# Kernel optimization log

Hardware: AMD Instinct MI355X
Metric: run time of the kernel (lower is better)

## Reference

```python
import jax, jax.numpy as jnp
import numpy as np

B, K, T, D, NH, HD, DFF, L = 2, 512, 2048, 1024, 16, 64, 4096, 2
EPS = 1e-5


def rotate_half(x):
    x1, x2 = jnp.split(x, 2, axis=-1)
    return jnp.concatenate([-x2, x1], axis=-1)


def rmsnorm(x, w):
    return x * jax.lax.rsqrt(jnp.mean(x * x, axis=-1, keepdims=True) + EPS) * w


def setup_inputs():
    key = jax.random.key(0)
    ks = jax.random.split(key, 16)
    x_processed = jax.random.normal(ks[0], (B, K, D), jnp.float32)
    # counts[b] = number of chunks n; boundaries[b, :n-1] = ascending chunk ends in (0, T),
    # positions >= n-1 padded with T (sentinel, never used by the original loop).
    counts = jax.random.randint(ks[1], (B,), K // 2, K + 1)
    raw = jnp.sort(jax.random.randint(ks[2], (B, K), 1, T), axis=1)
    j = jnp.arange(K)[None, :]
    boundaries = jnp.where(j < counts[:, None] - 1, raw, T)
    x_residual = jax.random.normal(ks[3], (B, T, D), jnp.float32)
    inv_freq = 1.0 / (10000.0 ** (jnp.arange(0, HD, 2, dtype=jnp.float32) / HD))
    freqs = jnp.arange(T, dtype=jnp.float32)[:, None] * inv_freq[None, :]  # [T, HD//2]
    emb = jnp.concatenate([freqs, freqs], axis=-1)                          # [T, HD]
    cos, sin = jnp.cos(emb), jnp.sin(emb)
    s = 0.02
    wq = jax.random.normal(ks[4], (L, D, D), jnp.float32) * s
    wk = jax.random.normal(ks[5], (L, D, D), jnp.float32) * s
    wv = jax.random.normal(ks[6], (L, D, D), jnp.float32) * s
    wo = jax.random.normal(ks[7], (L, D, D), jnp.float32) * s
    w1 = jax.random.normal(ks[8], (L, D, DFF), jnp.float32) * s
    w3 = jax.random.normal(ks[9], (L, D, DFF), jnp.float32) * s
    w2 = jax.random.normal(ks[10], (L, DFF, D), jnp.float32) * s
    attn_norm_w = jnp.ones((L, D), jnp.float32)
    mlp_norm_w = jnp.ones((L, D), jnp.float32)
    final_norm_w = jnp.ones((D,), jnp.float32)
    return {"x_processed": x_processed, "boundaries": boundaries, "counts": counts,
            "x_residual": x_residual, "cos": cos, "sin": sin, "seq_len": T,
            "wq": wq, "wk": wk, "wv": wv, "wo": wo,
            "attn_norm_w": attn_norm_w, "mlp_norm_w": mlp_norm_w,
            "w1": w1, "w3": w3, "w2": w2, "final_norm_w": final_norm_w}


def reference(x_processed, boundaries, counts, x_residual, cos, sin, seq_len,
              wq, wk, wv, wo, attn_norm_w, mlp_norm_w, w1, w3, w2, final_norm_w):
    Bn, Kn, Dn = x_processed.shape
    Tn = x_residual.shape[1]
    # Vectorized chunk expansion: token t belongs to chunk i = #{boundaries <= t}
    # (boundaries ascending; entries beyond n-1 are padded with seq_len so they never count).
    t = jnp.arange(Tn)
    idx = jax.vmap(lambda row: jnp.searchsorted(row, t, side='right'))(boundaries)  # [B, T]
    x = jnp.take_along_axis(x_processed, idx[:, :, None], axis=1) + x_residual     # [B, T, D]

    mask = jnp.tril(jnp.ones((Tn, Tn), dtype=bool))
    scale = 1.0 / jnp.sqrt(jnp.float32(HD))
    c = cos[None, :, None, :]
    s = sin[None, :, None, :]
    for l in range(L):
        h = rmsnorm(x, attn_norm_w[l])
        q = (h @ wq[l]).reshape(Bn, Tn, NH, HD)
        k = (h @ wk[l]).reshape(Bn, Tn, NH, HD)
        v = (h @ wv[l]).reshape(Bn, Tn, NH, HD)
        q = q * c + rotate_half(q) * s
        k = k * c + rotate_half(k) * s
        scores = jnp.einsum('bthd,bshd->bhts', q, k) * scale
        scores = jnp.where(mask[None, None], scores, -jnp.inf)
        probs = jax.nn.softmax(scores, axis=-1)
        o = jnp.einsum('bhts,bshd->bthd', probs, v).reshape(Bn, Tn, Dn)
        x = x + o @ wo[l]
        h = rmsnorm(x, mlp_norm_w[l])
        x = x + (jax.nn.silu(h @ w1[l]) * (h @ w3[l])) @ w2[l]
    return rmsnorm(x, final_norm_w)
```

## Files before the change

### kernel.cpp

```cpp
#include <hip/hip_runtime.h>
#include <stdint.h>

typedef __attribute__((ext_vector_type(8))) short s16x8;
typedef __attribute__((ext_vector_type(4))) float f32x4;

#define CB 2
#define CT 2048
#define CD 1024
#define CNH 16
#define CHD 64
#define CDFF 4096
#define CKB 512

__device__ __forceinline__ short f2bf(float f){
  union { float f; uint32_t u; } v; v.f = f;
  uint32_t r = v.u + 0x7FFFu + ((v.u >> 16) & 1u);
  return (short)(r >> 16);
}
__device__ __forceinline__ float bf2f(short h){
  union { uint32_t u; float f; } v; v.u = ((uint32_t)(uint16_t)h) << 16;
  return v.f;
}
__device__ __forceinline__ uint32_t cvtpk_bf16(float lo, float hi){
  uint32_t r;
  asm("v_cvt_pk_bf16_f32 %0, %1, %2" : "=v"(r) : "v"(lo), "v"(hi));
  return r;
}

#define GLOAD16(g, l) __builtin_amdgcn_global_load_lds( \
    (const __attribute__((address_space(1))) void*)(g), \
    (__attribute__((address_space(3))) void*)(l), 16, 0, 0)

__global__ void gather_kernel(const float* __restrict__ xp, const int* __restrict__ bnd,
                              const float* __restrict__ xr, float* __restrict__ x){
  int t = blockIdx.x, b = blockIdx.y, tid = threadIdx.x;
  int lo = 0, hi = CKB;
  while (lo < hi){ int mid = (lo + hi) >> 1; if (bnd[b*CKB + mid] <= t) lo = mid + 1; else hi = mid; }
  const float4* s  = (const float4*)(xp + ((size_t)b*CKB + lo)*CD);
  const float4* rr = (const float4*)(xr + ((size_t)b*CT + t)*CD);
  float4* dst      = (float4*)(x  + ((size_t)b*CT + t)*CD);
  float4 a = s[tid], c = rr[tid];
  float4 o; o.x = a.x + c.x; o.y = a.y + c.y; o.z = a.z + c.z; o.w = a.w + c.w;
  dst[tid] = o;
}

__global__ void wtrans_kernel(const float* __restrict__ W, short* __restrict__ dst,
                              int Kd, int Nd){
  __shared__ __align__(16) float tile[64*65];
  int n0 = blockIdx.x*64, k0 = blockIdx.y*64;
  #pragma unroll
  for (int i = 0; i < 16; ++i){
    int e = threadIdx.x + 256*i; int kl = e >> 6, nl = e & 63;
    tile[kl*65 + nl] = W[(size_t)(k0 + kl)*Nd + n0 + nl];
  }
  __syncthreads();
  #pragma unroll
  for (int i = 0; i < 16; ++i){
    int e = threadIdx.x + 256*i; int nl = e >> 6, kl = e & 63;
    dst[(size_t)(n0 + nl)*Kd + k0 + kl] = f2bf(tile[kl*65 + nl]);
  }
}

__global__ void wtrans_inter_kernel(const float* __restrict__ W, short* __restrict__ dst,
                                    int Kd, int Nd, int off16){
  __shared__ __align__(16) float tile[64*65];
  int n0 = blockIdx.x*64, k0 = blockIdx.y*64;
  #pragma unroll
  for (int i = 0; i < 16; ++i){
    int e = threadIdx.x + 256*i; int kl = e >> 6, nl = e & 63;
    tile[kl*65 + nl] = W[(size_t)(k0 + kl)*Nd + n0 + nl];
  }
  __syncthreads();
  #pragma unroll
  for (int i = 0; i < 16; ++i){
    int e = threadIdx.x + 256*i; int nl = e >> 6, kl = e & 63;
    int c = n0 + nl;
    int frow = ((c >> 4) << 5) + off16 + (c & 15);
    dst[(size_t)frow*Kd + k0 + kl] = f2bf(tile[kl*65 + nl]);
  }
}

template<int OUT_BF16>
__global__ void rmsnorm_kernel(const float* __restrict__ x, const float* __restrict__ w,
                               void* __restrict__ outv){
  int row = blockIdx.x, tid = threadIdx.x;
  const float4 xv = ((const float4*)(x + (size_t)row*CD))[tid];
  float ss = xv.x*xv.x + xv.y*xv.y + xv.z*xv.z + xv.w*xv.w;
  #pragma unroll
  for (int m = 1; m < 64; m <<= 1) ss += __shfl_xor(ss, m);
  __shared__ float red[4];
  if ((tid & 63) == 0) red[tid >> 6] = ss;
  __syncthreads();
  float tot = red[0] + red[1] + red[2] + red[3];
  float scale = rsqrtf(tot * (1.0f/1024.0f) + 1e-5f);
  const float4 wv = ((const float4*)w)[tid];
  if (OUT_BF16){
    short4 o;
    o.x = f2bf(xv.x*scale*wv.x); o.y = f2bf(xv.y*scale*wv.y);
    o.z = f2bf(xv.z*scale*wv.z); o.w = f2bf(xv.w*scale*wv.w);
    ((short4*)outv)[(size_t)row*256 + tid] = o;
  } else {
    float4 o;
    o.x = xv.x*scale*wv.x; o.y = xv.y*scale*wv.y;
    o.z = xv.z*scale*wv.z; o.w = xv.w*scale*wv.w;
    ((float4*)outv)[(size_t)row*256 + tid] = o;
  }
}

__device__ __forceinline__ void swz_block_id(int id, int NX, int NY, int& bm, int& bn){
  const int nwg = NX*NY;
  const int qq = nwg >> 3, rr8 = nwg & 7;
  const int xcd = id & 7, loc = id >> 3;
  const int wgid = (xcd < rr8 ? xcd*(qq+1) : rr8*(qq+1) + (xcd-rr8)*qq) + loc;
  const int GM = 8;
  const int gsz = GM * NX;
  const int gidg = wgid / gsz;
  const int remg = wgid - gidg*gsz;
  bm = gidg*GM + (remg % GM);
  bn = remg / GM;
}

template<int EPI>
__global__ __launch_bounds__(256) void gemm_bt(const short* __restrict__ A,
                                               const short* __restrict__ Bt,
                                               void* __restrict__ Cv,
                                               int M, int N, int K,
                                               int NX, int NY){
  __shared__ __align__(16) short sA[2][128*32];
  __shared__ __align__(16) short sB[2][128*32];
  const int tid = threadIdx.x;
  const int lane = tid & 63, wid = tid >> 6;
  const int wm = wid >> 1, wn = wid & 1;
  const int lr = lane & 15, lg = lane >> 4;
  int bm, bn; swz_block_id(blockIdx.x, NX, NY, bm, bn);
  const int bm0 = bm * 128, bn0 = bn * 128;

  f32x4 acc[4][4];
  #pragma unroll
  for (int i = 0; i < 4; ++i)
    #pragma unroll
    for (int j = 0; j < 4; ++j) acc[i][j] = (f32x4){0.f,0.f,0.f,0.f};

  const short* gA = A  + (size_t)(bm0 + wid*32 + (lane >> 2))*K + (lane & 3)*8;
  const short* gB = Bt + (size_t)(bn0 + wid*32 + (lane >> 2))*K + (lane & 3)*8;

  #pragma unroll
  for (int iss = 0; iss < 2; ++iss){
    GLOAD16(gA + (size_t)iss*16*K, &sA[0][wid*1024 + iss*16*32]);
    GLOAD16(gB + (size_t)iss*16*K, &sB[0][wid*1024 + iss*16*32]);
  }
  __syncthreads();

  int cur = 0;
  for (int k0 = 0; k0 < K; k0 += 32){
    if (k0 + 32 < K){
      #pragma unroll
      for (int iss = 0; iss < 2; ++iss){
        GLOAD16(gA + (size_t)iss*16*K + k0 + 32, &sA[cur^1][wid*1024 + iss*16*32]);
        GLOAD16(gB + (size_t)iss*16*K + k0 + 32, &sB[cur^1][wid*1024 + iss*16*32]);
      }
    }
    s16x8 af[4], bq[4];
    #pragma unroll
    for (int i = 0; i < 4; ++i) af[i] = *(const s16x8*)&sA[cur][(wm*64 + i*16 + lr)*32 + lg*8];
    #pragma unroll
    for (int j = 0; j < 4; ++j) bq[j] = *(const s16x8*)&sB[cur][(wn*64 + j*16 + lr)*32 + lg*8];
    #pragma unroll
    for (int i = 0; i < 4; ++i)
      #pragma unroll
      for (int j = 0; j < 4; ++j)
        acc[i][j] = __builtin_amdgcn_mfma_f32_16x16x32_bf16(af[i], bq[j], acc[i][j], 0, 0, 0);
    __syncthreads();
    cur ^= 1;
  }

  if (EPI == 0){
    short* C = (short*)Cv;
    #pragma unroll
    for (int i = 0; i < 4; ++i){
      int row0 = bm0 + wm*64 + i*16 + lg*4;
      #pragma unroll
      for (int j = 0; j < 4; ++j){
        int col = bn0 + wn*64 + j*16 + lr;
        #pragma unroll
        for (int r = 0; r < 4; ++r) C[(size_t)(row0 + r)*N + col] = f2bf(acc[i][j][r]);
      }
    }
  } else {
    float* C = (float*)Cv;
    #pragma unroll
    for (int i = 0; i < 4; ++i){
      int row0 = bm0 + wm*64 + i*16 + lg*4;
      #pragma unroll
      for (int j = 0; j < 4; ++j){
        int col = bn0 + wn*64 + j*16 + lr;
        #pragma unroll
        for (int r = 0; r < 4; ++r) C[(size_t)(row0 + r)*N + col] += acc[i][j][r];
      }
    }
  }
}

__global__ __launch_bounds__(256) void gemm_splitk(const short* __restrict__ A,
                                                   const short* __restrict__ Bt,
                                                   float* __restrict__ Cp,
                                                   int M, int N, int Ktot, int Kchunk,
                                                   int NX, int NY){
  __shared__ __align__(16) short sA[2][128*32];
  __shared__ __align__(16) short sB[2][128*32];
  const int tid = threadIdx.x;
  const int lane = tid & 63, wid = tid >> 6;
  const int wm = wid >> 1, wn = wid & 1;
  const int lr = lane & 15, lg = lane >> 4;
  const int nin = NX*NY;
  const int split = blockIdx.x / nin;
  const int inner = blockIdx.x - split*nin;
  int bm, bn; swz_block_id(inner, NX, NY, bm, bn);
  const int bm0 = bm * 128, bn0 = bn * 128;
  const int koff = split * Kchunk;

  f32x4 acc[4][4];
  #pragma unroll
  for (int i = 0; i < 4; ++i)
    #pragma unroll
    for (int j = 0; j < 4; ++j) acc[i][j] = (f32x4){0.f,0.f,0.f,0.f};

  const short* gA = A  + (size_t)(bm0 + wid*32 + (lane >> 2))*Ktot + koff + (lane & 3)*8;
  const short* gB = Bt + (size_t)(bn0 + wid*32 + (lane >> 2))*Ktot + koff + (lane & 3)*8;

  #pragma unroll
  for (int iss = 0; iss < 2; ++iss){
    GLOAD16(gA + (size_t)iss*16*Ktot, &sA[0][wid*1024 + iss*16*32]);
    GLOAD16(gB + (size_t)iss*16*Ktot, &sB[0][wid*1024 + iss*16*32]);
  }
  __syncthreads();

  int cur = 0;
  for (int k0 = 0; k0 < Kchunk; k0 += 32){
    if (k0 + 32 < Kchunk){
      #pragma unroll
      for (int iss = 0; iss < 2; ++iss){
        GLOAD16(gA + (size_t)iss*16*Ktot + k0 + 32, &sA[cur^1][wid*1024 + iss*16*32]);
        GLOAD16(gB + (size_t)iss*16*Ktot + k0 + 32, &sB[cur^1][wid*1024 + iss*16*32]);
      }
    }
    s16x8 af[4], bq[4];
    #pragma unroll
    for (int i = 0; i < 4; ++i) af[i] = *(const s16x8*)&sA[cur][(wm*64 + i*16 + lr)*32 + lg*8];
    #pragma unroll
    for (int j = 0; j < 4; ++j) bq[j] = *(const s16x8*)&sB[cur][(wn*64 + j*16 + lr)*32 + lg*8];
    #pragma unroll
    for (int i = 0; i < 4; ++i)
      #pragma unroll
      for (int j = 0; j < 4; ++j)
        acc[i][j] = __builtin_amdgcn_mfma_f32_16x16x32_bf16(af[i], bq[j], acc[i][j], 0, 0, 0);
    __syncthreads();
    cur ^= 1;
  }

  float* C = Cp + (size_t)split*M*N;
  #pragma unroll
  for (int i = 0; i < 4; ++i){
    int row0 = bm0 + wm*64 + i*16 + lg*4;
    #pragma unroll
    for (int j = 0; j < 4; ++j){
      int col = bn0 + wn*64 + j*16 + lr;
      #pragma unroll
      for (int r = 0; r < 4; ++r) C[(size_t)(row0 + r)*N + col] = acc[i][j][r];
    }
  }
}

__global__ void redadd_kernel(float* __restrict__ x, const float* __restrict__ Cp){
  size_t i = (size_t)blockIdx.x*256 + threadIdx.x;
  const float4* p0 = (const float4*)Cp;
  const float4* p1 = p0 + (size_t)1048576;
  const float4* p2 = p1 + (size_t)1048576;
  const float4* p3 = p2 + (size_t)1048576;
  float4 a = ((float4*)x)[i];
  float4 q0 = p0[i], q1 = p1[i], q2 = p2[i], q3 = p3[i];
  a.x += (q0.x + q1.x) + (q2.x + q3.x);
  a.y += (q0.y + q1.y) + (q2.y + q3.y);
  a.z += (q0.z + q1.z) + (q2.z + q3.z);
  a.w += (q0.w + q1.w) + (q2.w + q3.w);
  ((float4*)x)[i] = a;
}

#define STAGE8(u, kt, bufx) do { \
  const short* Gp_ = ((u)&1) ? Bt : A; \
  const int rb_ = ((u)&1) ? bn0 : bm0; \
  const int kh_ = (u)>>1; \
  _Pragma("unroll") \
  for (int L_ = 0; L_ < 2; ++L_){ \
    int rowS_ = L_*128 + wid*16 + (lane>>2); \
    int sp_ = (lane&3) ^ ((rowS_>>1)&3); \
    GLOAD16(Gp_ + (size_t)(rb_ + rowS_)*K + (size_t)(kt)*64 + kh_*32 + sp_*8, \
            &sAB[bufx][u][(L_*512 + wid*64)*8]); \
  } \
} while(0)

#define PHASE8(p, ch, kk) do { \
  if (pf) STAGE8(p, kt+1, nbuf); \
  s16x8 af_[4], bq_[4]; \
  _Pragma("unroll") \
  for (int ii_ = 0; ii_ < 4; ++ii_){ \
    int rowA_ = wm*128 + ((ch)*4 + ii_)*16 + lr; \
    af_[ii_] = *(const s16x8*)&sAB[buf][(kk)*2][rowA_*32 + ((lg ^ ((rowA_>>1)&3))<<3)]; \
  } \
  _Pragma("unroll") \
  for (int j_ = 0; j_ < 4; ++j_){ \
    int rowB_ = wn*64 + j_*16 + lr; \
    bq_[j_] = *(const s16x8*)&sAB[buf][(kk)*2+1][rowB_*32 + ((lg ^ ((rowB_>>1)&3))<<3)]; \
  } \
  __builtin_amdgcn_s_barrier(); \
  asm volatile("s_waitcnt lgkmcnt(0)" ::: "memory"); \
  __builtin_amdgcn_s_setprio(1); \
  _Pragma("unroll") \
  for (int ii_ = 0; ii_ < 4; ++ii_) \
    _Pragma("unroll") \
    for (int j_ = 0; j_ < 4; ++j_) \
      acc[(ch)*4 + ii_][j_] = __builtin_amdgcn_mfma_f32_16x16x32_bf16(af_[ii_], bq_[j_], acc[(ch)*4 + ii_][j_], 0, 0, 0); \
  __builtin_amdgcn_s_setprio(0); \
  if ((p) == 1){ \
    if (pf) asm volatile("s_waitcnt vmcnt(4)" ::: "memory"); \
    else    asm volatile("s_waitcnt vmcnt(0)" ::: "memory"); \
  } \
  if ((p) == 3 && pf) asm volatile("s_waitcnt vmcnt(4)" ::: "memory"); \
  __builtin_amdgcn_s_barrier(); \
} while(0)

template<int FUSE>
__global__ __launch_bounds__(512, 2) void gemm8p(const short* __restrict__ A,
                                                 const short* __restrict__ Bt,
                                                 short* __restrict__ C,
                                                 int M, int N, int K,
                                                 int NX, int NY){
  __shared__ __align__(16) short sAB[2][4][256*32];
  const int tid = threadIdx.x;
  const int lane = tid & 63, wid = tid >> 6;
  const int wm = wid >> 2, wn = wid & 3;
  const int lr = lane & 15, lg = lane >> 4;
  int bm, bn; swz_block_id(blockIdx.x, NX, NY, bm, bn);
  const int bm0 = bm * 256, bn0 = bn * 256;

  f32x4 acc[8][4];
  #pragma unroll
  for (int i = 0; i < 8; ++i)
    #pragma unroll
    for (int j = 0; j < 4; ++j) acc[i][j] = (f32x4){0.f,0.f,0.f,0.f};

  const int NK = K >> 6;
  STAGE8(0, 0, 0);
  STAGE8(1, 0, 0);
  STAGE8(2, 0, 0);
  STAGE8(3, 0, 0);
  asm volatile("s_waitcnt vmcnt(4)" ::: "memory");
  __builtin_amdgcn_s_barrier();

  #pragma unroll 1
  for (int kt = 0; kt < NK; ++kt){
    const bool pf = (kt + 1 < NK);
    const int buf = kt & 1, nbuf = buf ^ 1;
    PHASE8(0, 0, 0);
    PHASE8(1, 1, 0);
    PHASE8(2, 0, 1);
    PHASE8(3, 1, 1);
  }

  if (FUSE == 0){
    #pragma unroll
    for (int i = 0; i < 8; ++i){
      int row0 = bm0 + wm*128 + i*16 + lg*4;
      #pragma unroll
      for (int j = 0; j < 4; ++j){
        int col = bn0 + wn*64 + j*16 + lr;
        #pragma unroll
        for (int r = 0; r < 4; ++r) C[(size_t)(row0 + r)*N + col] = f2bf(acc[i][j][r]);
      }
    }
  } else {
    const int Nh = N >> 1;
    #pragma unroll
    for (int i = 0; i < 8; ++i){
      int row0 = bm0 + wm*128 + i*16 + lg*4;
      #pragma unroll
      for (int jp = 0; jp < 2; ++jp){
        int col = (bn0 >> 1) + wn*32 + jp*16 + lr;
        #pragma unroll
        for (int r = 0; r < 4; ++r){
          float u = acc[i][jp*2][r], g = acc[i][jp*2+1][r];
          float val = u / (1.f + __expf(-u)) * g;
          C[(size_t)(row0 + r)*Nh + col] = f2bf(val);
        }
      }
    }
  }
}

__global__ void rope_kernel(const short* __restrict__ qkv, const float* __restrict__ cosb,
                            const float* __restrict__ sinb, short* __restrict__ Qo,
                            short* __restrict__ Ko){
  int g = blockIdx.x*256 + threadIdx.x;
  int d = g & 31;
  int h = (g >> 5) & 15;
  int t = (g >> 9) & 2047;
  int b = g >> 20;
  size_t row = (size_t)b*CT + t;
  const short* src = qkv + row*3072 + h*64;
  float q0 = bf2f(src[d]),        q1 = bf2f(src[d+32]);
  float k0 = bf2f(src[1024+d]),   k1 = bf2f(src[1024+d+32]);
  float c0 = cosb[t*64 + d], c1 = cosb[t*64 + d + 32];
  float s0 = sinb[t*64 + d], s1 = sinb[t*64 + d + 32];
  size_t o = row*CD + h*64;
  const float sc = 0.125f * 1.44269504088896340736f;
  Qo[o + d]      = f2bf((q0*c0 - q1*s0)*sc);
  Qo[o + d + 32] = f2bf((q1*c1 + q0*s1)*sc);
  Ko[o + d]      = f2bf(k0*c0 - k1*s0);
  Ko[o + d + 32] = f2bf(k1*c1 + k0*s1);
}

__global__ void vtrans_kernel(const short* __restrict__ qkv, short* __restrict__ Vt){
  __shared__ __align__(16) short tile[64*65];
  int t0 = blockIdx.x*64;
  int h = blockIdx.y & 15, b = blockIdx.y >> 4;
  #pragma unroll
  for (int i = 0; i < 16; ++i){
    int e = threadIdx.x + 256*i; int tl = e >> 6, d = e & 63;
    tile[tl*65 + d] = qkv[(size_t)(b*CT + t0 + tl)*3072 + 2048 + h*64 + d];
  }
  __syncthreads();
  #pragma unroll
  for (int i = 0; i < 16; ++i){
    int e = threadIdx.x + 256*i; int dl = e >> 6, tl = e & 63;
    Vt[((size_t)(b*CNH + h)*CHD + dl)*CT + t0 + tl] = tile[tl*65 + dl];
  }
}

__global__ __launch_bounds__(256) void attn_kernel(const short* __restrict__ Q,
                                                   const short* __restrict__ Kb,
                                                   const short* __restrict__ Vt,
                                                   short* __restrict__ O){
  __shared__ __align__(16) short Kl[2][64*72];
  __shared__ __align__(16) short Vl[2][64*72];
  __shared__ __align__(16) short Pl[4][16*72];
  const int tid = threadIdx.x, lane = tid & 63, w = tid >> 6;
  const int qpair = blockIdx.x;
  const int h = blockIdx.y, b = blockIdx.z;
  const int lr = lane & 15, lg = lane >> 4;

  const short* gK = Kb + (size_t)b*CT*CD + h*CHD;
  const short* gV = Vt + (size_t)(b*CNH + h)*CHD*CT;
  const int srow0 = tid >> 3, scol = (tid & 7)*8;

  #pragma unroll 1
  for (int half = 0; half < 2; ++half){
    const int qt = half ? qpair : (31 - qpair);
    const int wq0 = qt*64 + w*16;
    const int jmax = qt + 1;

    s16x8 qf0, qf1;
    {
      const short* qp = Q + ((size_t)(b*CT + wq0 + lr)*CNH + h)*CHD + lg*8;
      qf0 = *(const s16x8*)qp;
      qf1 = *(const s16x8*)(qp + 32);
    }
    f32x4 oacc[4];
    #pragma unroll
    for (int dt = 0; dt < 4; ++dt) oacc[dt] = (f32x4){0.f,0.f,0.f,0.f};
    float m_r = -1e30f, l_r = 0.f;

    #pragma unroll
    for (int p = 0; p < 2; ++p){
      int row = srow0 + p*32;
      *(s16x8*)&Kl[0][row*72 + scol] = *(const s16x8*)(gK + (size_t)row*CD + scol);
      *(s16x8*)&Vl[0][row*72 + scol] = *(const s16x8*)(gV + (size_t)row*CT + scol);
    }
    __syncthreads();

    #pragma unroll 1
    for (int j = 0; j < jmax; ++j){
      const int kv0 = j*64;
      const int buf = j & 1;
      s16x8 nk[2], nv[2];
      const bool havenext = (j + 1 < jmax);
      if (havenext){
        const int kv1 = kv0 + 64;
        #pragma unroll
        for (int p = 0; p < 2; ++p){
          int row = srow0 + p*32;
          nk[p] = *(const s16x8*)(gK + (size_t)(kv1 + row)*CD + scol);
          nv[p] = *(const s16x8*)(gV + (size_t)row*CT + kv1 + scol);
        }
      }

      if (kv0 < wq0 + 16){
        f32x4 sc[4];
        __builtin_amdgcn_s_setprio(1);
        #pragma unroll
        for (int nt = 0; nt < 4; ++nt){
          s16x8 k0 = *(const s16x8*)&Kl[buf][(nt*16 + lr)*72 + lg*8];
          s16x8 k1 = *(const s16x8*)&Kl[buf][(nt*16 + lr)*72 + 32 + lg*8];
          f32x4 z = (f32x4){0.f,0.f,0.f,0.f};
          z = __builtin_amdgcn_mfma_f32_16x16x32_bf16(k0, qf0, z, 0, 0, 0);
          z = __builtin_amdgcn_mfma_f32_16x16x32_bf16(k1, qf1, z, 0, 0, 0);
          sc[nt] = z;
        }
        __builtin_amdgcn_s_setprio(0);
        if (kv0 + 64 > wq0){
          #pragma unroll
          for (int nt = 0; nt < 4; ++nt)
            #pragma unroll
            for (int r = 0; r < 4; ++r)
              if (kv0 + nt*16 + lg*4 + r > wq0 + lr) sc[nt][r] = -1e30f;
        }
        float pmax = sc[0][0];
        #pragma unroll
        for (int nt = 0; nt < 4; ++nt)
          #pragma unroll
          for (int r = 0; r < 4; ++r) pmax = fmaxf(pmax, sc[nt][r]);
        pmax = fmaxf(pmax, __shfl_xor(pmax, 16));
        pmax = fmaxf(pmax, __shfl_xor(pmax, 32));
        if (!__all(pmax - m_r <= 10.f)){
          float mn = fmaxf(m_r, pmax);
          float corr = __builtin_amdgcn_exp2f(m_r - mn);
          m_r = mn;
          l_r *= corr;
          #pragma unroll
          for (int r = 0; r < 4; ++r){
            float c4 = __shfl(corr, lg*4 + r);
            #pragma unroll
            for (int dt = 0; dt < 4; ++dt) oacc[dt][r] *= c4;
          }
        }
        float rs = 0.f;
        #pragma unroll
        for (int nt = 0; nt < 4; ++nt)
          #pragma unroll
          for (int r = 0; r < 4; ++r){
            float pv = __builtin_amdgcn_exp2f(sc[nt][r] - m_r);
            sc[nt][r] = pv;
            rs += pv;
          }
        #pragma unroll
        for (int nt = 0; nt < 4; ++nt){
          uint2 pk;
          pk.x = cvtpk_bf16(sc[nt][0], sc[nt][1]);
          pk.y = cvtpk_bf16(sc[nt][2], sc[nt][3]);
          *(uint2*)&Pl[w][lr*72 + nt*16 + lg*4] = pk;
        }
        rs += __shfl_xor(rs, 16);
        rs += __shfl_xor(rs, 32);
        l_r += rs;
        s16x8 pa0 = *(const s16x8*)&Pl[w][lr*72 + lg*8];
        s16x8 pa1 = *(const s16x8*)&Pl[w][lr*72 + 32 + lg*8];
        __builtin_amdgcn_s_setprio(1);
        #pragma unroll
        for (int dt = 0; dt < 4; ++dt){
          s16x8 v0 = *(const s16x8*)&Vl[buf][(dt*16 + lr)*72 + lg*8];
          s16x8 v1 = *(const s16x8*)&Vl[buf][(dt*16 + lr)*72 + 32 + lg*8];
          oacc[dt] = __builtin_amdgcn_mfma_f32_16x16x32_bf16(pa0, v0, oacc[dt], 0, 0, 0);
          oacc[dt] = __builtin_amdgcn_mfma_f32_16x16x32_bf16(pa1, v1, oacc[dt], 0, 0, 0);
        }
        __builtin_amdgcn_s_setprio(0);
      }
      if (havenext){
        #pragma unroll
        for (int p = 0; p < 2; ++p){
          int row = srow0 + p*32;
          *(s16x8*)&Kl[buf^1][row*72 + scol] = nk[p];
          *(s16x8*)&Vl[buf^1][row*72 + scol] = nv[p];
        }
      }
      __syncthreads();
    }

    #pragma unroll
    for (int r = 0; r < 4; ++r){
      float lf = __shfl(l_r, lg*4 + r);
      float inv = 1.f / lf;
      int qrow = wq0 + lg*4 + r;
      #pragma unroll
      for (int dt = 0; dt < 4; ++dt)
        O[((size_t)(b*CT + qrow)*CNH + h)*CHD + dt*16 + lr] = f2bf(oacc[dt][r] * inv);
    }
  }
}

extern "C" void kernel_launch(void* const* d_in, const int* in_sizes, int n_in,
                              void* d_out, int out_size, void* d_ws, size_t ws_size,
                              hipStream_t stream){
  (void)in_sizes; (void)n_in; (void)out_size; (void)ws_size;
  const float* x_processed = (const float*)d_in[0];
  const int*   boundaries  = (const int*)d_in[1];
  const float* x_residual  = (const float*)d_in[3];
  const float* cosb        = (const float*)d_in[4];
  const float* sinb        = (const float*)d_in[5];
  const float* wq          = (const float*)d_in[7];
  const float* wk          = (const float*)d_in[8];
  const float* wv          = (const float*)d_in[9];
  const float* wo          = (const float*)d_in[10];
  const float* attn_nw     = (const float*)d_in[11];
  const float* mlp_nw      = (const float*)d_in[12];
  const float* w1          = (const float*)d_in[13];
  const float* w3          = (const float*)d_in[14];
  const float* w2          = (const float*)d_in[15];
  const float* final_nw    = (const float*)d_in[16];

  char* p = (char*)d_ws;
  auto alloc = [&](size_t bytes)->char*{
    char* r = p; p += (bytes + 255) & ~(size_t)255; return r;
  };
  short* wqkvT = (short*)alloc((size_t)2*3072*1024*2);
  short* woT   = (short*)alloc((size_t)2*1024*1024*2);
  short* w13T  = (short*)alloc((size_t)2*8192*1024*2);
  short* w2T   = (short*)alloc((size_t)2*1024*4096*2);
  float* x     = (float*)alloc((size_t)4096*1024*4);
  short* hbuf  = (short*)alloc((size_t)4096*1024*2);
  short* qkv   = (short*)alloc((size_t)4096*3072*2);
  short* qr    = (short*)alloc((size_t)4096*1024*2);
  short* kr    = (short*)alloc((size_t)4096*1024*2);
  short* vt    = (short*)alloc((size_t)4096*1024*2);
  short* obuf  = (short*)alloc((size_t)4096*1024*2);
  short* mbuf  = (short*)alloc((size_t)4096*4096*2);
  float* psum  = (float*)alloc((size_t)4*4096*1024*4);

  for (int l = 0; l < 2; ++l){
    size_t wOff = (size_t)l*1024*1024;
    wtrans_kernel<<<dim3(16,16),256,0,stream>>>(wq + wOff, wqkvT + (size_t)l*3072*1024,                     1024, 1024);
    wtrans_kernel<<<dim3(16,16),256,0,stream>>>(wk + wOff, wqkvT + (size_t)l*3072*1024 + (size_t)1024*1024, 1024, 1024);
    wtrans_kernel<<<dim3(16,16),256,0,stream>>>(wv + wOff, wqkvT + (size_t)l*3072*1024 + (size_t)2048*1024, 1024, 1024);
    wtrans_kernel<<<dim3(16,16),256,0,stream>>>(wo + wOff, woT + (size_t)l*1024*1024,                       1024, 1024);
    wtrans_inter_kernel<<<dim3(64,16),256,0,stream>>>(w1 + (size_t)l*1024*4096, w13T + (size_t)l*8192*1024, 1024, 4096, 0);
    wtrans_inter_kernel<<<dim3(64,16),256,0,stream>>>(w3 + (size_t)l*1024*4096, w13T + (size_t)l*8192*1024, 1024, 4096, 16);
    wtrans_kernel<<<dim3(16,64),256,0,stream>>>(w2 + (size_t)l*4096*1024, w2T + (size_t)l*1024*4096,        4096, 1024);
  }
  gather_kernel<<<dim3(2048,2),256,0,stream>>>(x_processed, boundaries, x_residual, x);
  for (int l = 0; l < 2; ++l){
    rmsnorm_kernel<1><<<4096,256,0,stream>>>(x, attn_nw + l*1024, hbuf);
    gemm8p<0><<<12*16,512,0,stream>>>(hbuf, wqkvT + (size_t)l*3072*1024, qkv, 4096, 3072, 1024, 12, 16);
    rope_kernel<<<8192,256,0,stream>>>(qkv, cosb, sinb, qr, kr);
    vtrans_kernel<<<dim3(32,32),256,0,stream>>>(qkv, vt);
    attn_kernel<<<dim3(16,16,2),256,0,stream>>>(qr, kr, vt, obuf);
    gemm_bt<1><<<8*32,256,0,stream>>>(obuf, woT + (size_t)l*1024*1024, x, 4096, 1024, 1024, 8, 32);
    rmsnorm_kernel<1><<<4096,256,0,stream>>>(x, mlp_nw + l*1024, hbuf);
    gemm8p<1><<<32*16,512,0,stream>>>(hbuf, w13T + (size_t)l*8192*1024, mbuf, 4096, 8192, 1024, 32, 16);
    gemm_splitk<<<8*32*4,256,0,stream>>>(mbuf, w2T + (size_t)l*1024*4096, psum, 4096, 1024, 4096, 1024, 8, 32);
    redadd_kernel<<<4096,256,0,stream>>>(x, psum);
  }
  rmsnorm_kernel<0><<<4096,256,0,stream>>>(x, final_nw, d_out);
}
```

Before: 646.4 us.

## Route W2 split-K through gemm8p and fuse reduction with following RMSNorm

The down-projection now runs through the larger 256x256 gemm8p kernel with split-K support, replacing the separate 128x128 split-K GEMM. The split-K reduction is fused with the next RMSNorm (the next layer's attention norm, or the final norm), so one launch and one full pass over x are removed per layer. The gemm8p inner phases are also regrouped into paired stages, with both K-halves' prefetches issued together and A fragments loaded once per pair. The down-projection grid shrinks to 256 blocks, which may lower occupancy for that GEMM.

```diff
diff --git a/kernel.cpp b/kernel.cpp
--- a/kernel.cpp
+++ b/kernel.cpp
@@ -107,6 +107,44 @@
   }
 }
 
+template<int OUT_BF16>
+__global__ void redrms_kernel(float* __restrict__ x, const float* __restrict__ Cp,
+                              const float* __restrict__ w, void* __restrict__ outv){
+  int row = blockIdx.x, tid = threadIdx.x;
+  size_t i = (size_t)row*256 + tid;
+  const float4* p0 = (const float4*)Cp;
+  const float4* p1 = p0 + (size_t)1048576;
+  const float4* p2 = p1 + (size_t)1048576;
+  const float4* p3 = p2 + (size_t)1048576;
+  float4 a = ((float4*)x)[i];
+  float4 q0 = p0[i], q1 = p1[i], q2 = p2[i], q3 = p3[i];
+  a.x += (q0.x + q1.x) + (q2.x + q3.x);
+  a.y += (q0.y + q1.y) + (q2.y + q3.y);
+  a.z += (q0.z + q1.z) + (q2.z + q3.z);
+  a.w += (q0.w + q1.w) + (q2.w + q3.w);
+  if (OUT_BF16) ((float4*)x)[i] = a;
+  float ss = a.x*a.x + a.y*a.y + a.z*a.z + a.w*a.w;
+  #pragma unroll
+  for (int m = 1; m < 64; m <<= 1) ss += __shfl_xor(ss, m);
+  __shared__ float red[4];
+  if ((tid & 63) == 0) red[tid >> 6] = ss;
+  __syncthreads();
+  float tot = red[0] + red[1] + red[2] + red[3];
+  float scale = rsqrtf(tot * (1.0f/1024.0f) + 1e-5f);
+  const float4 wv = ((const float4*)w)[tid];
+  if (OUT_BF16){
+    short4 o;
+    o.x = f2bf(a.x*scale*wv.x); o.y = f2bf(a.y*scale*wv.y);
+    o.z = f2bf(a.z*scale*wv.z); o.w = f2bf(a.w*scale*wv.w);
+    ((short4*)outv)[(size_t)row*256 + tid] = o;
+  } else {
+    float4 o;
+    o.x = a.x*scale*wv.x; o.y = a.y*scale*wv.y;
+    o.z = a.z*scale*wv.z; o.w = a.w*scale*wv.w;
+    ((float4*)outv)[(size_t)row*256 + tid] = o;
+  }
+}
+
 __device__ __forceinline__ void swz_block_id(int id, int NX, int NY, int& bm, int& bn){
   const int nwg = NX*NY;
   const int qq = nwg >> 3, rr8 = nwg & 7;
@@ -201,91 +239,6 @@
   }
 }
 
-__global__ __launch_bounds__(256) void gemm_splitk(const short* __restrict__ A,
-                                                   const short* __restrict__ Bt,
-                                                   float* __restrict__ Cp,
-                                                   int M, int N, int Ktot, int Kchunk,
-                                                   int NX, int NY){
-  __shared__ __align__(16) short sA[2][128*32];
-  __shared__ __align__(16) short sB[2][128*32];
-  const int tid = threadIdx.x;
-  const int lane = tid & 63, wid = tid >> 6;
-  const int wm = wid >> 1, wn = wid & 1;
-  const int lr = lane & 15, lg = lane >> 4;
-  const int nin = NX*NY;
-  const int split = blockIdx.x / nin;
-  const int inner = blockIdx.x - split*nin;
-  int bm, bn; swz_block_id(inner, NX, NY, bm, bn);
-  const int bm0 = bm * 128, bn0 = bn * 128;
-  const int koff = split * Kchunk;
-
-  f32x4 acc[4][4];
-  #pragma unroll
-  for (int i = 0; i < 4; ++i)
-    #pragma unroll
-    for (int j = 0; j < 4; ++j) acc[i][j] = (f32x4){0.f,0.f,0.f,0.f};
-
-  const short* gA = A  + (size_t)(bm0 + wid*32 + (lane >> 2))*Ktot + koff + (lane & 3)*8;
-  const short* gB = Bt + (size_t)(bn0 + wid*32 + (lane >> 2))*Ktot + koff + (lane & 3)*8;
-
-  #pragma unroll
-  for (int iss = 0; iss < 2; ++iss){
-    GLOAD16(gA + (size_t)iss*16*Ktot, &sA[0][wid*1024 + iss*16*32]);
-    GLOAD16(gB + (size_t)iss*16*Ktot, &sB[0][wid*1024 + iss*16*32]);
-  }
-  __syncthreads();
-
-  int cur = 0;
-  for (int k0 = 0; k0 < Kchunk; k0 += 32){
-    if (k0 + 32 < Kchunk){
-      #pragma unroll
-      for (int iss = 0; iss < 2; ++iss){
-        GLOAD16(gA + (size_t)iss*16*Ktot + k0 + 32, &sA[cur^1][wid*1024 + iss*16*32]);
-        GLOAD16(gB + (size_t)iss*16*Ktot + k0 + 32, &sB[cur^1][wid*1024 + iss*16*32]);
-      }
-    }
-    s16x8 af[4], bq[4];
-    #pragma unroll
-    for (int i = 0; i < 4; ++i) af[i] = *(const s16x8*)&sA[cur][(wm*64 + i*16 + lr)*32 + lg*8];
-    #pragma unroll
-    for (int j = 0; j < 4; ++j) bq[j] = *(const s16x8*)&sB[cur][(wn*64 + j*16 + lr)*32 + lg*8];
-    #pragma unroll
-    for (int i = 0; i < 4; ++i)
-      #pragma unroll
-      for (int j = 0; j < 4; ++j)
-        acc[i][j] = __builtin_amdgcn_mfma_f32_16x16x32_bf16(af[i], bq[j], acc[i][j], 0, 0, 0);
-    __syncthreads();
-    cur ^= 1;
-  }
-
-  float* C = Cp + (size_t)split*M*N;
-  #pragma unroll
-  for (int i = 0; i < 4; ++i){
-    int row0 = bm0 + wm*64 + i*16 + lg*4;
-    #pragma unroll
-    for (int j = 0; j < 4; ++j){
-      int col = bn0 + wn*64 + j*16 + lr;
-      #pragma unroll
-      for (int r = 0; r < 4; ++r) C[(size_t)(row0 + r)*N + col] = acc[i][j][r];
-    }
-  }
-}
-
-__global__ void redadd_kernel(float* __restrict__ x, const float* __restrict__ Cp){
-  size_t i = (size_t)blockIdx.x*256 + threadIdx.x;
-  const float4* p0 = (const float4*)Cp;
-  const float4* p1 = p0 + (size_t)1048576;
-  const float4* p2 = p1 + (size_t)1048576;
-  const float4* p3 = p2 + (size_t)1048576;
-  float4 a = ((float4*)x)[i];
-  float4 q0 = p0[i], q1 = p1[i], q2 = p2[i], q3 = p3[i];
-  a.x += (q0.x + q1.x) + (q2.x + q3.x);
-  a.y += (q0.y + q1.y) + (q2.y + q3.y);
-  a.z += (q0.z + q1.z) + (q2.z + q3.z);
-  a.w += (q0.w + q1.w) + (q2.w + q3.w);
-  ((float4*)x)[i] = a;
-}
-
 #define STAGE8(u, kt, bufx) do { \
   const short* Gp_ = ((u)&1) ? Bt : A; \
   const int rb_ = ((u)&1) ? bn0 : bm0; \
@@ -294,54 +247,60 @@
   for (int L_ = 0; L_ < 2; ++L_){ \
     int rowS_ = L_*128 + wid*16 + (lane>>2); \
     int sp_ = (lane&3) ^ ((rowS_>>1)&3); \
-    GLOAD16(Gp_ + (size_t)(rb_ + rowS_)*K + (size_t)(kt)*64 + kh_*32 + sp_*8, \
+    GLOAD16(Gp_ + (size_t)(rb_ + rowS_)*Kstr + (size_t)(kt)*64 + kh_*32 + sp_*8, \
             &sAB[bufx][u][(L_*512 + wid*64)*8]); \
   } \
 } while(0)
 
-#define PHASE8(p, ch, kk) do { \
-  if (pf) STAGE8(p, kt+1, nbuf); \
-  s16x8 af_[4], bq_[4]; \
+#define LDSRD(bufx, u, rowv) \
+  (*(const s16x8*)&sAB[bufx][u][(rowv)*32 + (((lg) ^ (((rowv)>>1)&3))<<3)])
+
+#define PHASEPAIR(kk) do { \
+  if (pf){ STAGE8(2*(kk), kt+1, nbuf); STAGE8(2*(kk)+1, kt+1, nbuf); } \
+  s16x8 af0_[4], af1_[4], bq_[4]; \
   _Pragma("unroll") \
-  for (int ii_ = 0; ii_ < 4; ++ii_){ \
-    int rowA_ = wm*128 + ((ch)*4 + ii_)*16 + lr; \
-    af_[ii_] = *(const s16x8*)&sAB[buf][(kk)*2][rowA_*32 + ((lg ^ ((rowA_>>1)&3))<<3)]; \
-  } \
+  for (int j_ = 0; j_ < 4; ++j_) bq_[j_] = LDSRD(buf, (kk)*2+1, wn*64 + j_*16 + lr); \
   _Pragma("unroll") \
-  for (int j_ = 0; j_ < 4; ++j_){ \
-    int rowB_ = wn*64 + j_*16 + lr; \
-    bq_[j_] = *(const s16x8*)&sAB[buf][(kk)*2+1][rowB_*32 + ((lg ^ ((rowB_>>1)&3))<<3)]; \
-  } \
+  for (int i_ = 0; i_ < 4; ++i_) af0_[i_] = LDSRD(buf, (kk)*2, wm*128 + i_*16 + lr); \
+  _Pragma("unroll") \
+  for (int i_ = 0; i_ < 4; ++i_) af1_[i_] = LDSRD(buf, (kk)*2, wm*128 + 64 + i_*16 + lr); \
   __builtin_amdgcn_s_barrier(); \
   asm volatile("s_waitcnt lgkmcnt(0)" ::: "memory"); \
   __builtin_amdgcn_s_setprio(1); \
   _Pragma("unroll") \
-  for (int ii_ = 0; ii_ < 4; ++ii_) \
+  for (int i_ = 0; i_ < 4; ++i_) \
     _Pragma("unroll") \
     for (int j_ = 0; j_ < 4; ++j_) \
-      acc[(ch)*4 + ii_][j_] = __builtin_amdgcn_mfma_f32_16x16x32_bf16(af_[ii_], bq_[j_], acc[(ch)*4 + ii_][j_], 0, 0, 0); \
+      acc[i_][j_] = __builtin_amdgcn_mfma_f32_16x16x32_bf16(af0_[i_], bq_[j_], acc[i_][j_], 0, 0, 0); \
+  _Pragma("unroll") \
+  for (int i_ = 0; i_ < 4; ++i_) \
+    _Pragma("unroll") \
+    for (int j_ = 0; j_ < 4; ++j_) \
+      acc[4+i_][j_] = __builtin_amdgcn_mfma_f32_16x16x32_bf16(af1_[i_], bq_[j_], acc[4+i_][j_], 0, 0, 0); \
   __builtin_amdgcn_s_setprio(0); \
-  if ((p) == 1){ \
-    if (pf) asm volatile("s_waitcnt vmcnt(4)" ::: "memory"); \
-    else    asm volatile("s_waitcnt vmcnt(0)" ::: "memory"); \
-  } \
-  if ((p) == 3 && pf) asm volatile("s_waitcnt vmcnt(4)" ::: "memory"); \
+  if (pf) asm volatile("s_waitcnt vmcnt(4)" ::: "memory"); \
+  else if ((kk) == 0) asm volatile("s_waitcnt vmcnt(0)" ::: "memory"); \
   __builtin_amdgcn_s_barrier(); \
 } while(0)
 
 template<int FUSE>
 __global__ __launch_bounds__(512, 2) void gemm8p(const short* __restrict__ A,
                                                  const short* __restrict__ Bt,
-                                                 short* __restrict__ C,
-                                                 int M, int N, int K,
+                                                 void* __restrict__ Cv,
+                                                 int M, int N, int Kstr, int Kchunk,
                                                  int NX, int NY){
   __shared__ __align__(16) short sAB[2][4][256*32];
   const int tid = threadIdx.x;
   const int lane = tid & 63, wid = tid >> 6;
   const int wm = wid >> 2, wn = wid & 3;
   const int lr = lane & 15, lg = lane >> 4;
-  int bm, bn; swz_block_id(blockIdx.x, NX, NY, bm, bn);
+  const int nin = NX*NY;
+  const int split = blockIdx.x / nin;
+  const int inner = blockIdx.x - split*nin;
+  int bm, bn; swz_block_id(inner, NX, NY, bm, bn);
   const int bm0 = bm * 256, bn0 = bn * 256;
+  A  += (size_t)split * Kchunk;
+  Bt += (size_t)split * Kchunk;
 
   f32x4 acc[8][4];
   #pragma unroll
@@ -349,7 +308,7 @@
     #pragma unroll
     for (int j = 0; j < 4; ++j) acc[i][j] = (f32x4){0.f,0.f,0.f,0.f};
 
-  const int NK = K >> 6;
+  const int NK = Kchunk >> 6;
   STAGE8(0, 0, 0);
   STAGE8(1, 0, 0);
   STAGE8(2, 0, 0);
@@ -361,13 +320,12 @@
   for (int kt = 0; kt < NK; ++kt){
     const bool pf = (kt + 1 < NK);
     const int buf = kt & 1, nbuf = buf ^ 1;
-    PHASE8(0, 0, 0);
-    PHASE8(1, 1, 0);
-    PHASE8(2, 0, 1);
-    PHASE8(3, 1, 1);
+    PHASEPAIR(0);
+    PHASEPAIR(1);
   }
 
   if (FUSE == 0){
+    short* C = (short*)Cv;
     #pragma unroll
     for (int i = 0; i < 8; ++i){
       int row0 = bm0 + wm*128 + i*16 + lg*4;
@@ -378,7 +336,8 @@
         for (int r = 0; r < 4; ++r) C[(size_t)(row0 + r)*N + col] = f2bf(acc[i][j][r]);
       }
     }
-  } else {
+  } else if (FUSE == 1){
+    short* C = (short*)Cv;
     const int Nh = N >> 1;
     #pragma unroll
     for (int i = 0; i < 8; ++i){
@@ -392,6 +351,18 @@
           float val = u / (1.f + __expf(-u)) * g;
           C[(size_t)(row0 + r)*Nh + col] = f2bf(val);
         }
+      }
+    }
+  } else {
+    float* C = (float*)Cv + (size_t)split*M*N;
+    #pragma unroll
+    for (int i = 0; i < 8; ++i){
+      int row0 = bm0 + wm*128 + i*16 + lg*4;
+      #pragma unroll
+      for (int j = 0; j < 4; ++j){
+        int col = bn0 + wn*64 + j*16 + lr;
+        #pragma unroll
+        for (int r = 0; r < 4; ++r) C[(size_t)(row0 + r)*N + col] = acc[i][j][r];
       }
     }
   }
@@ -635,17 +606,17 @@
     wtrans_kernel<<<dim3(16,64),256,0,stream>>>(w2 + (size_t)l*4096*1024, w2T + (size_t)l*1024*4096,        4096, 1024);
   }
   gather_kernel<<<dim3(2048,2),256,0,stream>>>(x_processed, boundaries, x_residual, x);
+  rmsnorm_kernel<1><<<4096,256,0,stream>>>(x, attn_nw, hbuf);
   for (int l = 0; l < 2; ++l){
-    rmsnorm_kernel<1><<<4096,256,0,stream>>>(x, attn_nw + l*1024, hbuf);
-    gemm8p<0><<<12*16,512,0,stream>>>(hbuf, wqkvT + (size_t)l*3072*1024, qkv, 4096, 3072, 1024, 12, 16);
+    gemm8p<0><<<12*16,512,0,stream>>>(hbuf, wqkvT + (size_t)l*3072*1024, qkv, 4096, 3072, 1024, 1024, 12, 16);
     rope_kernel<<<8192,256,0,stream>>>(qkv, cosb, sinb, qr, kr);
     vtrans_kernel<<<dim3(32,32),256,0,stream>>>(qkv, vt);
     attn_kernel<<<dim3(16,16,2),256,0,stream>>>(qr, kr, vt, obuf);
     gemm_bt<1><<<8*32,256,0,stream>>>(obuf, woT + (size_t)l*1024*1024, x, 4096, 1024, 1024, 8, 32);
     rmsnorm_kernel<1><<<4096,256,0,stream>>>(x, mlp_nw + l*1024, hbuf);
-    gemm8p<1><<<32*16,512,0,stream>>>(hbuf, w13T + (size_t)l*8192*1024, mbuf, 4096, 8192, 1024, 32, 16);
-    gemm_splitk<<<8*32*4,256,0,stream>>>(mbuf, w2T + (size_t)l*1024*4096, psum, 4096, 1024, 4096, 1024, 8, 32);
-    redadd_kernel<<<4096,256,0,stream>>>(x, psum);
-  }
-  rmsnorm_kernel<0><<<4096,256,0,stream>>>(x, final_nw, d_out);
-}
+    gemm8p<1><<<32*16,512,0,stream>>>(hbuf, w13T + (size_t)l*8192*1024, mbuf, 4096, 8192, 1024, 1024, 32, 16);
+    gemm8p<2><<<4*4*16,512,0,stream>>>(mbuf, w2T + (size_t)l*1024*4096, psum, 4096, 1024, 4096, 1024, 4, 16);
+    if (l == 0) redrms_kernel<1><<<4096,256,0,stream>>>(x, psum, attn_nw + 1024, hbuf);
+    else        redrms_kernel<0><<<4096,256,0,stream>>>(x, psum, final_nw, d_out);
+  }
+}
```

After: 618.1 us. -4.4%, faster.
